# Performance work log

Measured on AMD Instinct MI355X. Metric: run time of the kernel, lower is better.

## Reference

```python
import jax, jax.numpy as jnp
import numpy as np
import math

HIDDEN = 1024

def setup_inputs() -> dict:
    key = jax.random.key(0)
    k1, k2, k3, k4, k5 = jax.random.split(key, 5)
    s = 1.0 / math.sqrt(HIDDEN)
    return {
        "x": jax.random.normal(k1, (4, 2048, HIDDEN), dtype=jnp.float32),
        "W_qkv": jax.random.uniform(k2, (HIDDEN, 3 * HIDDEN), jnp.float32, -s, s),
        "b_qkv": jax.random.uniform(k3, (3 * HIDDEN,), jnp.float32, -s, s),
        "W_out": jax.random.uniform(k4, (HIDDEN, HIDDEN), jnp.float32, -s, s),
        "b_out": jax.random.uniform(k5, (HIDDEN,), jnp.float32, -s, s),
    }

def reference(x, W_qkv, b_qkv, W_out, b_out):
    # fused QKV projection: [b, s, 3h]
    qkv = jnp.einsum("bsh,hd->bsd", x, W_qkv) + b_qkv
    q, k, v = jnp.split(qkv, 3, axis=-1)
    scale = 1.0 / math.sqrt(x.shape[-1])
    scores = jnp.einsum("bqh,bkh->bqk", q, k) * scale  # [b, s, s]
    attn = jax.nn.softmax(scores, axis=-1)
    out = jnp.einsum("bqk,bkh->bqh", attn, v)
    return jnp.einsum("bsh,hd->bsd", out, W_out) + b_out
```

## Files before the change

kernel.cpp:

```cpp
#include <hip/hip_runtime.h>
#include <cstdint>
#include <cstddef>


typedef __bf16 bf16;
typedef __bf16 bf16x8 __attribute__((ext_vector_type(8)));
typedef __bf16 bf16x4 __attribute__((ext_vector_type(4)));
typedef float  f32x4  __attribute__((ext_vector_type(4)));

#define UNIT 8192

__device__ __forceinline__ void gload_lds16(const bf16* g, bf16* l) {
  __builtin_amdgcn_global_load_lds(
      (const __attribute__((address_space(1))) unsigned int*)g,
      (__attribute__((address_space(3))) unsigned int*)l, 16, 0, 0);
}

#define GATE(N)  asm volatile("s_waitcnt vmcnt(" #N ")" ::: "memory")
#define LGKM0()  asm volatile("s_waitcnt lgkmcnt(0)" ::: "memory")
#define SBAR()   __builtin_amdgcn_s_barrier()
#define SCHED0() __builtin_amdgcn_sched_barrier(0)

#define BK97 32
#define U97  4096

__device__ __forceinline__ void stage97(const bf16* g0, long ld, bf16* u, int tid) {
  const int wv = tid >> 6;
  #pragma unroll
  for (int j = 0; j < 2; ++j) {
    const int c = j * 256 + tid;
    const int r = c >> 2, s = c & 3;
    const int sg = s ^ ((r >> 1) & 3);
    const int cb = j * 256 + (wv << 6);
    gload_lds16(g0 + (long)r * ld + sg * 8, u + (size_t)cb * 8);
  }
}

__device__ __forceinline__ bf16x8 rd97(const bf16* u, int r, int s) {
  return *(const bf16x8*)(u + (size_t)r * 32 + (size_t)((s ^ ((r >> 1) & 3)) * 8));
}

template <int MODE>
__device__ __forceinline__ void gemm97_body(
    const bf16* __restrict__ A, long sAz, int lda,
    const bf16* __restrict__ B, long sBz, int ldb, int K,
    bf16* __restrict__ p0, long sCz, bf16* __restrict__ p1, bf16* __restrict__ p2,
    float* __restrict__ fout, const float* __restrict__ bias, float scale) {
  __shared__ bf16 lds[3][2][U97];
  const int tid = threadIdx.x;
  const int wv = tid >> 6, ln = tid & 63;
  const int wr = wv >> 1, wc = wv & 1;
  const int lr = ln & 15, lh = ln >> 4;
  const int m0 = blockIdx.x * 128, n0 = blockIdx.y * 128;
  const int z = blockIdx.z;
  const bf16* Ag = A + (long)z * sAz + (long)m0 * lda;
  const bf16* Bg = B + (long)z * sBz + (long)n0 * ldb;
  const int NT = K / BK97;

  stage97(Ag,        lda, &lds[0][0][0], tid);
  stage97(Bg,        ldb, &lds[0][1][0], tid);
  stage97(Ag + BK97, lda, &lds[1][0][0], tid);
  stage97(Bg + BK97, ldb, &lds[1][1][0], tid);
  GATE(4);
  SCHED0();
  SBAR();

  f32x4 acc[4][4];
  #pragma unroll
  for (int i = 0; i < 4; ++i)
    #pragma unroll
    for (int j = 0; j < 4; ++j) acc[i][j] = f32x4{0.f, 0.f, 0.f, 0.f};

  int rs = 0, ns = 2;
  for (int t = 0; t < NT; ++t) {
    const bf16* Au = &lds[rs][0][0];
    const bf16* Bu = &lds[rs][1][0];
    const bool pf = (t + 2 < NT);
    bf16x8 aF[4], bF[4];
    #pragma unroll
    for (int i = 0; i < 4; ++i) aF[i] = rd97(Au, wr * 64 + i * 16 + lr, lh);
    #pragma unroll
    for (int j = 0; j < 4; ++j) bF[j] = rd97(Bu, wc * 64 + j * 16 + lr, lh);
    if (pf) {
      stage97(Ag + (long)(t + 2) * BK97, lda, &lds[ns][0][0], tid);
      stage97(Bg + (long)(t + 2) * BK97, ldb, &lds[ns][1][0], tid);
    }
    LGKM0();
    SCHED0();
    __builtin_amdgcn_s_setprio(1);
    #pragma unroll
    for (int i = 0; i < 4; ++i)
      #pragma unroll
      for (int j = 0; j < 4; ++j)
        acc[i][j] = __builtin_amdgcn_mfma_f32_16x16x32_bf16(aF[i], bF[j], acc[i][j], 0, 0, 0);
    __builtin_amdgcn_s_setprio(0);
    if (t + 1 < NT) {
      if (pf) { GATE(4); } else { GATE(0); }
      SCHED0();
      SBAR();
    }
    rs = (rs == 2) ? 0 : rs + 1;
    ns = (ns == 2) ? 0 : ns + 1;
  }

  #pragma unroll
  for (int mf = 0; mf < 4; ++mf) {
    #pragma unroll
    for (int nf = 0; nf < 4; ++nf) {
      #pragma unroll
      for (int rg = 0; rg < 4; ++rg) {
        const int gm = m0 + wr * 64 + mf * 16 + lh * 4 + rg;
        const int gn = n0 + wc * 64 + nf * 16 + lr;
        float v = acc[mf][nf][rg];
        if constexpr (MODE == 0) {
          v += bias[gn];
          if (gn < 1024)       p0[(size_t)gm * 1024 + gn] = (bf16)v;
          else if (gn < 2048)  p1[(size_t)gm * 1024 + (gn - 1024)] = (bf16)v;
          else                 p2[(size_t)gm * 1024 + (gn - 2048)] = (bf16)v;
        } else if constexpr (MODE == 2) {
          p0[(size_t)z * sCz + (size_t)gm * 1024 + gn] = (bf16)v;
        } else {
          fout[(size_t)gm * 1024 + gn] = v + bias[gn];
        }
      }
    }
  }
}

#define GEMM_ARGS const bf16* A, long sAz, int lda, const bf16* B, long sBz, int ldb, \
                  int K, bf16* p0, long sCz, bf16* p1, bf16* p2, float* fout,         \
                  const float* bias, float scale
__global__ __launch_bounds__(256, 3) void gemm_qkv(GEMM_ARGS) {
  gemm97_body<0>(A, sAz, lda, B, sBz, ldb, K, p0, sCz, p1, p2, fout, bias, scale);
}
__global__ __launch_bounds__(256, 3) void gemm_pv(GEMM_ARGS) {
  gemm97_body<2>(A, sAz, lda, B, sBz, ldb, K, p0, sCz, p1, p2, fout, bias, scale);
}
__global__ __launch_bounds__(256, 3) void gemm_out(GEMM_ARGS) {
  gemm97_body<3>(A, sAz, lda, B, sBz, ldb, K, p0, sCz, p1, p2, fout, bias, scale);
}

#define THREADS8 512

__device__ __forceinline__ void stage_unit(const bf16* g0, long ld, bf16* ldsu, int tid) {
  const int wv = tid >> 6;
  #pragma unroll
  for (int j = 0; j < 2; ++j) {
    const int c = j * 512 + tid;
    const int r = c >> 3;
    const int sg = (c & 7) ^ (r & 7);
    const int cb = j * 512 + (wv << 6);
    gload_lds16(g0 + (long)r * ld + sg * 8, ldsu + (size_t)cb * 8);
  }
}

__device__ __forceinline__ bf16x8 rd_frag(const bf16* unitb, int r, int s) {
  return *(const bf16x8*)(unitb + (size_t)r * 64 + (size_t)((s ^ (r & 7)) * 8));
}

#define PHASE(DB, MH, NH, RA, RB, STAGE_CODE, GATE_CODE)                         \
  {                                                                              \
    if (RA) {                                                                    \
      _Pragma("unroll") for (int mf = 0; mf < 4; ++mf)                           \
        _Pragma("unroll") for (int ks = 0; ks < 2; ++ks)                         \
          aF[mf][ks] = rd_frag(&lds[DB][MH][0], wsm * 64 + mf * 16 + lr, ks * 4 + lh); \
    }                                                                            \
    if (RB) {                                                                    \
      _Pragma("unroll") for (int nf = 0; nf < 2; ++nf)                           \
        _Pragma("unroll") for (int ks = 0; ks < 2; ++ks)                         \
          bF[NH][nf][ks] = rd_frag(&lds[DB][2 + NH][0], wsn * 32 + nf * 16 + lr, ks * 4 + lh); \
    }                                                                            \
    STAGE_CODE;                                                                  \
    SBAR();                                                                      \
    LGKM0();                                                                     \
    SCHED0();                                                                    \
    __builtin_amdgcn_s_setprio(1);                                               \
    _Pragma("unroll") for (int mf = 0; mf < 4; ++mf)                             \
      _Pragma("unroll") for (int nf = 0; nf < 2; ++nf)                           \
        _Pragma("unroll") for (int ks = 0; ks < 2; ++ks)                         \
          acc[(MH)*4 + mf][(NH)*2 + nf] = __builtin_amdgcn_mfma_f32_16x16x32_bf16( \
              aF[mf][ks], bF[NH][nf][ks], acc[(MH)*4 + mf][(NH)*2 + nf], 0, 0, 0); \
    __builtin_amdgcn_s_setprio(0);                                               \
    GATE_CODE;                                                                   \
    SBAR();                                                                      \
    SCHED0();                                                                    \
  }

__global__ __launch_bounds__(THREADS8, 2) void gemm_sc(
    const bf16* __restrict__ A, long sAz, int lda,
    const bf16* __restrict__ B, long sBz, int ldb, int K,
    bf16* __restrict__ p0, long sCz, float scale) {
  __shared__ bf16 lds[2][4][UNIT];
  const int tid = threadIdx.x;
  const int wv = tid >> 6, ln = tid & 63;
  const int wsm = wv >> 2, wsn = wv & 3;
  const int lr = ln & 15, lh = ln >> 4;

  const int gx = gridDim.x, gy = gridDim.y;
  const int lin = blockIdx.x + gx * (blockIdx.y + gy * blockIdx.z);
  const int nwg = gx * gy * gridDim.z;
  const int swz = (lin & 7) * (nwg >> 3) + (lin >> 3);
  const int by = swz % gy;
  const int t2 = swz / gy;
  const int bx = t2 % gx;
  const int z  = t2 / gx;

  const int m0 = bx * 256, n0 = by * 256;
  const bf16* Ag = A + (long)z * sAz + (long)m0 * lda;
  const bf16* Bg = B + (long)z * sBz + (long)n0 * ldb;
  const int NITER = K / 128;

  stage_unit(Ag,             lda, &lds[0][0][0], tid);
  stage_unit(Bg,             ldb, &lds[0][2][0], tid);
  stage_unit(Ag + 128 * lda, lda, &lds[0][1][0], tid);
  stage_unit(Bg + 128 * ldb, ldb, &lds[0][3][0], tid);
  stage_unit(Ag + 64,        lda, &lds[1][0][0], tid);
  stage_unit(Bg + 64,        ldb, &lds[1][2][0], tid);
  GATE(8);
  SBAR();
  SCHED0();

  f32x4 acc[8][4];
  #pragma unroll
  for (int i = 0; i < 8; ++i)
    #pragma unroll
    for (int j = 0; j < 4; ++j) acc[i][j] = f32x4{0.f, 0.f, 0.f, 0.f};
  bf16x8 aF[4][2], bF[2][2][2];

  for (int it = 0; it < NITER; ++it) {
    const bool nl = (it + 1 < NITER);
    const long ktA = 2L * it + 1, ktB = 2L * it + 2, ktC = 2L * it + 3;
    PHASE(0, 0, 0, 1, 1,
      { stage_unit(Ag + 128 * lda + ktA * 64, lda, &lds[1][1][0], tid); },
      { GATE(6); });
    PHASE(0, 0, 1, 0, 1,
      { stage_unit(Bg + 128 * ldb + ktA * 64, ldb, &lds[1][3][0], tid); },
      { GATE(10); });
    PHASE(0, 1, 0, 1, 0,
      { if (nl) stage_unit(Ag + ktB * 64, lda, &lds[0][0][0], tid); },
      {});
    PHASE(0, 1, 1, 0, 0,
      { if (nl) stage_unit(Bg + ktB * 64, ldb, &lds[0][2][0], tid); },
      { if (nl) { GATE(8); } else { GATE(4); } });
    PHASE(1, 0, 0, 1, 1,
      { if (nl) stage_unit(Ag + 128 * lda + ktB * 64, lda, &lds[0][1][0], tid); },
      { if (nl) { GATE(6); } else { GATE(0); } });
    PHASE(1, 0, 1, 0, 1,
      { if (nl) stage_unit(Bg + 128 * ldb + ktB * 64, ldb, &lds[0][3][0], tid); },
      { GATE(10); });
    PHASE(1, 1, 0, 1, 0,
      { if (nl) stage_unit(Ag + ktC * 64, lda, &lds[1][0][0], tid); },
      {});
    PHASE(1, 1, 1, 0, 0,
      { if (nl) stage_unit(Bg + ktC * 64, ldb, &lds[1][2][0], tid); },
      { GATE(8); });
  }

  #pragma unroll
  for (int mi = 0; mi < 8; ++mi) {
    #pragma unroll
    for (int ni = 0; ni < 4; ++ni) {
      #pragma unroll
      for (int rg = 0; rg < 4; ++rg) {
        const int gm = m0 + (mi >> 2) * 128 + wsm * 64 + (mi & 3) * 16 + lh * 4 + rg;
        const int gn = n0 + (ni >> 1) * 128 + wsn * 32 + (ni & 1) * 16 + lr;
        p0[(size_t)z * sCz + (size_t)gm * 2048 + gn] = (bf16)(acc[mi][ni][rg] * scale);
      }
    }
  }
}

__global__ __launch_bounds__(256) void k_f32_to_bf16(const float* __restrict__ in,
                                                     bf16* __restrict__ out, long n) {
  long i = ((long)blockIdx.x * blockDim.x + threadIdx.x) * 4;
  if (i + 3 < n) {
    float4 v = *(const float4*)(in + i);
    bf16x4 o;
    o[0] = (bf16)v.x; o[1] = (bf16)v.y; o[2] = (bf16)v.z; o[3] = (bf16)v.w;
    *(bf16x4*)(out + i) = o;
  }
}

__global__ __launch_bounds__(256) void k_transpose(const float* __restrict__ in,
                                                   bf16* __restrict__ out, int R, int C) {
  __shared__ float t[32][33];
  int c0 = blockIdx.x * 32, r0 = blockIdx.y * 32;
  int tx = threadIdx.x, ty = threadIdx.y;
  #pragma unroll
  for (int dy = 0; dy < 32; dy += 8)
    t[ty + dy][tx] = in[(size_t)(r0 + ty + dy) * C + c0 + tx];
  __syncthreads();
  #pragma unroll
  for (int dy = 0; dy < 32; dy += 8)
    out[(size_t)(c0 + ty + dy) * R + r0 + tx] = (bf16)t[tx][ty + dy];
}

__global__ __launch_bounds__(256) void k_transpose_v(const bf16* __restrict__ in,
                                                     bf16* __restrict__ out) {
  __shared__ bf16 t[64][65];
  const int z = blockIdx.z;
  in  += (size_t)z * 2048 * 1024;
  out += (size_t)z * 1024 * 2048;
  int h0 = blockIdx.x * 64, s0 = blockIdx.y * 64;
  int tx = threadIdx.x, ty = threadIdx.y;
  #pragma unroll
  for (int dy = 0; dy < 64; dy += 4)
    t[ty + dy][tx] = in[(size_t)(s0 + ty + dy) * 1024 + h0 + tx];
  __syncthreads();
  #pragma unroll
  for (int dy = 0; dy < 64; dy += 4)
    out[(size_t)(h0 + ty + dy) * 2048 + s0 + tx] = t[tx][ty + dy];
}

__global__ __launch_bounds__(256) void k_softmax(bf16* __restrict__ S) {
  const int row = blockIdx.x;
  bf16* p = S + (size_t)row * 2048;
  const int tid = threadIdx.x;
  bf16x8 vin = *(const bf16x8*)(p + tid * 8);
  float x[8];
  float mx = -1e30f;
  #pragma unroll
  for (int i = 0; i < 8; ++i) { x[i] = (float)vin[i]; mx = fmaxf(mx, x[i]); }
  #pragma unroll
  for (int off = 32; off; off >>= 1) mx = fmaxf(mx, __shfl_down(mx, off));
  __shared__ float redm[4];
  if ((tid & 63) == 0) redm[tid >> 6] = mx;
  __syncthreads();
  mx = fmaxf(fmaxf(redm[0], redm[1]), fmaxf(redm[2], redm[3]));
  float s = 0.f;
  #pragma unroll
  for (int i = 0; i < 8; ++i) { x[i] = __expf(x[i] - mx); s += x[i]; }
  #pragma unroll
  for (int off = 32; off; off >>= 1) s += __shfl_down(s, off);
  __shared__ float reds[4];
  if ((tid & 63) == 0) reds[tid >> 6] = s;
  __syncthreads();
  s = reds[0] + reds[1] + reds[2] + reds[3];
  float inv = 1.0f / s;
  bf16x8 vo;
  #pragma unroll
  for (int i = 0; i < 8; ++i) vo[i] = (bf16)(x[i] * inv);
  *(bf16x8*)(p + tid * 8) = vo;
}

extern "C" void kernel_launch(void* const* d_in, const int* in_sizes, int n_in,
                              void* d_out, int out_size, void* d_ws, size_t ws_size,
                              hipStream_t stream) {
  const float* x    = (const float*)d_in[0];
  const float* Wqkv = (const float*)d_in[1];
  const float* bqkv = (const float*)d_in[2];
  const float* Wout = (const float*)d_in[3];
  const float* bout = (const float*)d_in[4];
  float* out = (float*)d_out;

  char* w = (char*)d_ws;
  const size_t MB = 1ull << 20;
  bf16* Xb  = (bf16*)(w);
  bf16* WqT = (bf16*)(w + 16 * MB);
  bf16* WoT = (bf16*)(w + 22 * MB);
  bf16* Qb  = (bf16*)(w + 24 * MB);
  bf16* Kb  = (bf16*)(w + 40 * MB);
  bf16* Vb  = (bf16*)(w + 56 * MB);
  bf16* Sb  = (bf16*)(w + 72 * MB);
  bf16* AO  = (bf16*)(w + 104 * MB);
  bf16* VT  = Xb;

  k_f32_to_bf16<<<8192, 256, 0, stream>>>(x, Xb, 8388608L);
  dim3 tb(32, 8);
  k_transpose<<<dim3(96, 32), tb, 0, stream>>>(Wqkv, WqT, 1024, 3072);
  k_transpose<<<dim3(32, 32), tb, 0, stream>>>(Wout, WoT, 1024, 1024);

  gemm_qkv<<<dim3(64, 24), 256, 0, stream>>>(
      Xb, 0L, 1024, WqT, 0L, 1024, 1024, Qb, 0L, Kb, Vb, nullptr, bqkv, 1.0f);

  k_transpose_v<<<dim3(16, 32, 4), dim3(64, 4), 0, stream>>>(Vb, VT);

  gemm_sc<<<dim3(8, 8, 4), THREADS8, 0, stream>>>(
      Qb, 2048L * 1024, 1024, Kb, 2048L * 1024, 1024, 1024,
      Sb, 2048L * 2048, 0.03125f);

  k_softmax<<<8192, 256, 0, stream>>>(Sb);

  gemm_pv<<<dim3(16, 8, 4), 256, 0, stream>>>(
      Sb, 2048L * 2048, 2048, VT, 1024L * 2048, 2048, 2048,
      AO, 2048L * 1024, nullptr, nullptr, nullptr, nullptr, 1.0f);

  gemm_out<<<dim3(64, 8), 256, 0, stream>>>(
      AO, 0L, 1024, WoT, 0L, 1024, 1024,
      nullptr, 0L, nullptr, nullptr, out, bout, 1.0f);
}
```

Baseline: 212.8 us.

## Reassociate attention output projection as P·(V·W_out) to drop V transpose

Measured after the change: 209.9 us. No clear change (-1.4%).

```diff
diff --git a/kernel.cpp b/kernel.cpp
--- a/kernel.cpp
+++ b/kernel.cpp
@@ -44,8 +44,10 @@
 __device__ __forceinline__ void gemm97_body(
     const bf16* __restrict__ A, long sAz, int lda,
     const bf16* __restrict__ B, long sBz, int ldb, int K,
-    bf16* __restrict__ p0, long sCz, bf16* __restrict__ p1, bf16* __restrict__ p2,
-    float* __restrict__ fout, const float* __restrict__ bias, float scale) {
+    bf16* __restrict__ p0, long sCz, int ldc,
+    bf16* __restrict__ p1, bf16* __restrict__ p2,
+    float* __restrict__ fout, long sFz,
+    const float* __restrict__ bias, float scale) {
   __shared__ bf16 lds[3][2][U97];
   const int tid = threadIdx.x;
   const int wv = tid >> 6, ln = tid & 63;
@@ -118,9 +120,9 @@
           else if (gn < 2048)  p1[(size_t)gm * 1024 + (gn - 1024)] = (bf16)v;
           else                 p2[(size_t)gm * 1024 + (gn - 2048)] = (bf16)v;
         } else if constexpr (MODE == 2) {
-          p0[(size_t)z * sCz + (size_t)gm * 1024 + gn] = (bf16)v;
+          p0[(size_t)z * sCz + (size_t)gm * ldc + gn] = (bf16)(v * scale);
         } else {
-          fout[(size_t)gm * 1024 + gn] = v + bias[gn];
+          fout[(size_t)z * sFz + (size_t)gm * ldc + gn] = v + bias[gn];
         }
       }
     }
@@ -128,16 +130,16 @@
 }
 
 #define GEMM_ARGS const bf16* A, long sAz, int lda, const bf16* B, long sBz, int ldb, \
-                  int K, bf16* p0, long sCz, bf16* p1, bf16* p2, float* fout,         \
-                  const float* bias, float scale
+                  int K, bf16* p0, long sCz, int ldc, bf16* p1, bf16* p2,             \
+                  float* fout, long sFz, const float* bias, float scale
 __global__ __launch_bounds__(256, 3) void gemm_qkv(GEMM_ARGS) {
-  gemm97_body<0>(A, sAz, lda, B, sBz, ldb, K, p0, sCz, p1, p2, fout, bias, scale);
-}
-__global__ __launch_bounds__(256, 3) void gemm_pv(GEMM_ARGS) {
-  gemm97_body<2>(A, sAz, lda, B, sBz, ldb, K, p0, sCz, p1, p2, fout, bias, scale);
-}
-__global__ __launch_bounds__(256, 3) void gemm_out(GEMM_ARGS) {
-  gemm97_body<3>(A, sAz, lda, B, sBz, ldb, K, p0, sCz, p1, p2, fout, bias, scale);
+  gemm97_body<0>(A, sAz, lda, B, sBz, ldb, K, p0, sCz, ldc, p1, p2, fout, sFz, bias, scale);
+}
+__global__ __launch_bounds__(256, 3) void gemm_vwt(GEMM_ARGS) {
+  gemm97_body<2>(A, sAz, lda, B, sBz, ldb, K, p0, sCz, ldc, p1, p2, fout, sFz, bias, scale);
+}
+__global__ __launch_bounds__(256, 3) void gemm_pvw(GEMM_ARGS) {
+  gemm97_body<3>(A, sAz, lda, B, sBz, ldb, K, p0, sCz, ldc, p1, p2, fout, sFz, bias, scale);
 }
 
 #define THREADS8 512
@@ -295,23 +297,6 @@
     out[(size_t)(c0 + ty + dy) * R + r0 + tx] = (bf16)t[tx][ty + dy];
 }
 
-__global__ __launch_bounds__(256) void k_transpose_v(const bf16* __restrict__ in,
-                                                     bf16* __restrict__ out) {
-  __shared__ bf16 t[64][65];
-  const int z = blockIdx.z;
-  in  += (size_t)z * 2048 * 1024;
-  out += (size_t)z * 1024 * 2048;
-  int h0 = blockIdx.x * 64, s0 = blockIdx.y * 64;
-  int tx = threadIdx.x, ty = threadIdx.y;
-  #pragma unroll
-  for (int dy = 0; dy < 64; dy += 4)
-    t[ty + dy][tx] = in[(size_t)(s0 + ty + dy) * 1024 + h0 + tx];
-  __syncthreads();
-  #pragma unroll
-  for (int dy = 0; dy < 64; dy += 4)
-    out[(size_t)(h0 + ty + dy) * 2048 + s0 + tx] = t[tx][ty + dy];
-}
-
 __global__ __launch_bounds__(256) void k_softmax(bf16* __restrict__ S) {
   const int row = blockIdx.x;
   bf16* p = S + (size_t)row * 2048;
@@ -362,8 +347,7 @@
   bf16* Kb  = (bf16*)(w + 40 * MB);
   bf16* Vb  = (bf16*)(w + 56 * MB);
   bf16* Sb  = (bf16*)(w + 72 * MB);
-  bf16* AO  = (bf16*)(w + 104 * MB);
-  bf16* VT  = Xb;
+  bf16* VWT = (bf16*)(w + 104 * MB);
 
   k_f32_to_bf16<<<8192, 256, 0, stream>>>(x, Xb, 8388608L);
   dim3 tb(32, 8);
@@ -371,9 +355,12 @@
   k_transpose<<<dim3(32, 32), tb, 0, stream>>>(Wout, WoT, 1024, 1024);
 
   gemm_qkv<<<dim3(64, 24), 256, 0, stream>>>(
-      Xb, 0L, 1024, WqT, 0L, 1024, 1024, Qb, 0L, Kb, Vb, nullptr, bqkv, 1.0f);
-
-  k_transpose_v<<<dim3(16, 32, 4), dim3(64, 4), 0, stream>>>(Vb, VT);
+      Xb, 0L, 1024, WqT, 0L, 1024, 1024,
+      Qb, 0L, 1024, Kb, Vb, nullptr, 0L, bqkv, 1.0f);
+
+  gemm_vwt<<<dim3(8, 16, 4), 256, 0, stream>>>(
+      WoT, 0L, 1024, Vb, 2048L * 1024, 1024, 1024,
+      VWT, 1024L * 2048, 2048, nullptr, nullptr, nullptr, 0L, nullptr, 1.0f);
 
   gemm_sc<<<dim3(8, 8, 4), THREADS8, 0, stream>>>(
       Qb, 2048L * 1024, 1024, Kb, 2048L * 1024, 1024, 1024,
@@ -381,11 +368,7 @@
 
   k_softmax<<<8192, 256, 0, stream>>>(Sb);
 
-  gemm_pv<<<dim3(16, 8, 4), 256, 0, stream>>>(
-      Sb, 2048L * 2048, 2048, VT, 1024L * 2048, 2048, 2048,
-      AO, 2048L * 1024, nullptr, nullptr, nullptr, nullptr, 1.0f);
-
-  gemm_out<<<dim3(64, 8), 256, 0, stream>>>(
-      AO, 0L, 1024, WoT, 0L, 1024, 1024,
-      nullptr, 0L, nullptr, nullptr, out, bout, 1.0f);
-}
+  gemm_pvw<<<dim3(16, 8, 4), 256, 0, stream>>>(
+      Sb, 2048L * 2048, 2048, VWT, 1024L * 2048, 2048, 2048,
+      nullptr, 0L, 1024, nullptr, nullptr, out, 2048L * 1024, bout, 1.0f);
+}
```
